# Kernel optimization log

Measured on AMD Instinct MI355X. Metric: run time of the kernel, lower is better.

Reference implementation:

```python
import jax, jax.numpy as jnp
import numpy as np

B, T, DIN, D = 32, 2048, 512, 512


def setup_inputs() -> dict:
    key = jax.random.key(0)
    k0, k1, k2, k3 = jax.random.split(key, 4)
    x = jax.random.normal(k0, (B, T, DIN), dtype=jnp.float32)
    h0 = jax.random.normal(k1, (B, D), dtype=jnp.float32)
    s0 = jax.random.normal(k2, (B, D), dtype=jnp.float32)
    # nn.Linear(input_dim, 6*hidden_dim): weight [6D, DIN], bias [6D]
    W = jax.random.normal(k3, (6 * D, DIN), dtype=jnp.float32) / np.float32(np.sqrt(DIN))
    b = jnp.zeros((6 * D,), dtype=jnp.float32)
    return {"x": x, "h0": h0, "s0": s0, "W": W, "b": b}


def reference(x, h0, s0, W, b):
    # Fused input projection for all 6 gates, done once as a big GEMM: [B,T,6D]
    proj = jnp.einsum("bti,oi->bto", x, W) + b
    proj = jnp.transpose(proj, (1, 0, 2))  # [T, B, 6D] for scan over time
    sig = jax.nn.sigmoid

    def step(carry, z):
        h, s = carry  # each [B, D]
        z0, z1, z2, z3, z4, z5 = jnp.split(z, 6, axis=-1)
        # gated two-state recurrence (6 gates, input-only projection,
        # elementwise recurrence on h/s as in the fused Triton cell)
        s_new = sig(z0) * s + sig(z1) * jnp.tanh(z2)
        h_new = sig(z3) * h + sig(z4) * jnp.tanh(z5 + s_new)
        return (h_new, s_new), h_new

    (hT, sT), hs = jax.lax.scan(step, (h0, s0), proj)
    out = jnp.transpose(hs, (1, 0, 2))  # [B, T, D]
    return out, sT
```

## Files before the change

kernel.cpp:

```cpp
#include <hip/hip_runtime.h>
#include <hip/hip_bf16.h>
#include <cstddef>
#include <cstdint>

#define BB   32
#define TT   2048
#define DIN  512
#define DD   512
#define NN   3072
#define PW   3072
#define PF   16

#define BMT 256
#define BNT 256
#define BKT 32
#define NKT (DIN / BKT)

typedef __attribute__((ext_vector_type(4))) float f32x4;
typedef __attribute__((ext_vector_type(8))) short s16x8;

__device__ __forceinline__ void gl2lds16(const void* g, void* l) {
    __builtin_amdgcn_global_load_lds(
        (const __attribute__((address_space(1))) unsigned*)g,
        (__attribute__((address_space(3))) unsigned*)l, 16, 0, 0);
}

__device__ __forceinline__ unsigned short bfr(float f) {
    unsigned u = __float_as_uint(f);
    u += 0x7fffu + ((u >> 16) & 1u);
    return (unsigned short)(u >> 16);
}

__device__ __forceinline__ float ftanh(float x) {
    return 1.f - 2.f * __builtin_amdgcn_rcpf(1.f + __builtin_amdgcn_exp2f(x * 2.885390082f));
}

__device__ __forceinline__ float h2lo(unsigned u) {
    return (float)__builtin_bit_cast(_Float16, (unsigned short)(u & 0xffffu));
}
__device__ __forceinline__ float h2hi(unsigned u) {
    return (float)__builtin_bit_cast(_Float16, (unsigned short)(u >> 16));
}

__global__ __launch_bounds__(256) void convert_x(
    const float* __restrict__ x, unsigned short* __restrict__ x2)
{
    const int total4 = BB * TT * DIN / 4;
    for (int idx = blockIdx.x * 256 + threadIdx.x; idx < total4;
         idx += gridDim.x * 256) {
        int e = idx * 4;
        int b = e >> 20;
        int t = (e >> 9) & 2047;
        int i = e & 511;
        float4 v = *(const float4*)(x + (size_t)e);
        ushort4 o;
        o.x = bfr(v.x); o.y = bfr(v.y); o.z = bfr(v.z); o.w = bfr(v.w);
        *(ushort4*)(x2 + ((size_t)((t << 5) | b) << 9) + i) = o;
    }
}

__global__ __launch_bounds__(128) void convert_w(
    const float* __restrict__ W, const float* __restrict__ bias,
    unsigned short* __restrict__ W2, float* __restrict__ bias2)
{
    int c = blockIdx.x;
    int p = c >> 10, d = (c & 1023) >> 1, q = c & 1;
    int o = ((2 * p + q) << 9) + d;
    const float* src = W + (size_t)o * DIN;
    unsigned short* dst = W2 + (size_t)c * DIN;
    int i = threadIdx.x * 4;
    float4 v = *(const float4*)(src + i);
    ushort4 u;
    u.x = bfr(v.x); u.y = bfr(v.y); u.z = bfr(v.z); u.w = bfr(v.w);
    *(ushort4*)(dst + i) = u;
    if (threadIdx.x == 0) bias2[c] = bias[o];
}

__global__ __launch_bounds__(512, 2) void gemm_proj10(
    const unsigned short* __restrict__ x2,
    const unsigned short* __restrict__ W2,
    const float* __restrict__ bias2,
    _Float16* __restrict__ proj,
    int t0)
{
    __shared__ unsigned short lds[3 * 16384];

    const unsigned nwg = gridDim.x;
    const unsigned fb  = blockIdx.x;
    const unsigned qq  = nwg >> 3, rr8 = nwg & 7;
    const unsigned xcd = fb & 7, sid = fb >> 3;
    const unsigned work = (xcd < rr8 ? xcd * (qq + 1)
                                     : rr8 * (qq + 1) + (xcd - rr8) * qq) + sid;
    const int bx = (int)(work % (NN / BNT));
    const int by = (int)(work / (NN / BNT));

    const int tid  = threadIdx.x;
    const int row0 = by * BMT;
    const int col0 = bx * BNT;
    const size_t growA = (size_t)t0 * BB + row0;

    const int lane = tid & 63;
    const int wv   = tid >> 6;
    const int wm   = wv >> 2;
    const int wn   = wv & 3;
    const int lr   = lane & 15;
    const int lq   = lane >> 4;

    auto stageA = [&](int s, int kt) {
        unsigned short* Ab = lds + s * 16384;
        const int k0 = kt * BKT;
        #pragma unroll
        for (int a = 0; a < 2; ++a) {
            int cid = a * 512 + tid;
            int rt  = cid >> 2;
            int cp  = cid & 3;
            gl2lds16(x2 + (growA + rt) * DIN + k0 + cp * 8, Ab + cid * 8);
        }
    };
    auto stageB = [&](int s, int kt) {
        unsigned short* Bb = lds + s * 16384 + 8192;
        const int k0 = kt * BKT;
        #pragma unroll
        for (int a = 0; a < 2; ++a) {
            int cid = a * 512 + tid;
            int rt  = cid >> 2;
            int cp  = cid & 3;
            gl2lds16(W2 + (size_t)(col0 + rt) * DIN + k0 + cp * 8, Bb + cid * 8);
        }
    };

    f32x4 acc[8][4] = {};

    stageA(0, 0); stageB(0, 0);
    stageA(1, 1); stageB(1, 1);
    asm volatile("s_waitcnt vmcnt(4)" ::: "memory");
    __builtin_amdgcn_s_barrier();

    #pragma unroll
    for (int kt = 0; kt < NKT; ++kt) {
        const unsigned short* Ab = lds + (kt % 3) * 16384;
        const unsigned short* Bb = Ab + 8192;
        const int  ks = (kt + 2) % 3;
        const bool st = (kt + 2) < NKT;

        if (st) { stageA(ks, kt + 2); stageB(ks, kt + 2); }

        s16x8 bv[4], av[8];
        #pragma unroll
        for (int j = 0; j < 4; ++j) {
            int col = wn * 64 + j * 16 + lr;
            bv[j] = *(const s16x8*)(Bb + col * BKT + lq * 8);
        }
        #pragma unroll
        for (int m = 0; m < 8; ++m) {
            int row = wm * 128 + m * 16 + lr;
            av[m] = *(const s16x8*)(Ab + row * BKT + lq * 8);
        }

        __builtin_amdgcn_s_setprio(1);
        #pragma unroll
        for (int m = 0; m < 8; ++m)
            #pragma unroll
            for (int j = 0; j < 4; ++j)
                acc[m][j] = __builtin_amdgcn_mfma_f32_16x16x32_bf16(
                    bv[j], av[m], acc[m][j], 0, 0, 0);
        __builtin_amdgcn_s_setprio(0);

        if (kt + 1 < NKT) {
            if (st) asm volatile("s_waitcnt vmcnt(4)" ::: "memory");
            else    asm volatile("s_waitcnt vmcnt(0)" ::: "memory");
            __builtin_amdgcn_s_barrier();
        }
    }

    const int p = col0 >> 10;
    const bool evenTanh = (p == 1);
    const bool oddIdent = (p == 2);
    const float mEven = evenTanh ? 2.885390082f : -1.442695041f;

    #pragma unroll
    for (int m = 0; m < 8; ++m) {
        int prow = row0 + wm * 128 + m * 16 + lr;
        _Float16* dst = proj + (size_t)prow * PW;
        #pragma unroll
        for (int j = 0; j < 4; ++j) {
            int cbase = col0 + wn * 64 + j * 16 + lq * 4;
            float4 bc = *(const float4*)(bias2 + cbase);
            float z0 = acc[m][j][0] + bc.x;
            float z1 = acc[m][j][1] + bc.y;
            float z2 = acc[m][j][2] + bc.z;
            float z3 = acc[m][j][3] + bc.w;
            float e0 = __builtin_amdgcn_rcpf(1.f + __builtin_amdgcn_exp2f(z0 * mEven));
            float e2 = __builtin_amdgcn_rcpf(1.f + __builtin_amdgcn_exp2f(z2 * mEven));
            float v0 = evenTanh ? (1.f - 2.f * e0) : e0;
            float v2 = evenTanh ? (1.f - 2.f * e2) : e2;
            float v1 = oddIdent ? z1
                : __builtin_amdgcn_rcpf(1.f + __builtin_amdgcn_exp2f(z1 * -1.442695041f));
            float v3 = oddIdent ? z3
                : __builtin_amdgcn_rcpf(1.f + __builtin_amdgcn_exp2f(z3 * -1.442695041f));
            ushort4 o;
            o.x = __builtin_bit_cast(unsigned short, (_Float16)v0);
            o.y = __builtin_bit_cast(unsigned short, (_Float16)v1);
            o.z = __builtin_bit_cast(unsigned short, (_Float16)v2);
            o.w = __builtin_bit_cast(unsigned short, (_Float16)v3);
            *(ushort4*)(dst + cbase) = o;
        }
    }
}

__global__ __launch_bounds__(64) void scan_chunk(
    const _Float16* __restrict__ proj,
    const float* __restrict__ h0, const float* __restrict__ s0,
    float* __restrict__ outH, float* __restrict__ outS,
    int t0, int Tc)
{
    const int gid = blockIdx.x * 64 + threadIdx.x;
    const int b   = gid >> 9;
    const int d   = gid & 511;

    float h, s;
    if (t0 == 0) { h = h0[gid]; s = s0[gid]; }
    else {
        h = outH[((size_t)b * TT + (t0 - 1)) * DD + d];
        s = outS[gid];
    }

    const unsigned* pu = (const unsigned*)(proj + (size_t)b * PW + d * 2);
    const size_t tstr = (size_t)BB * PW / 2;
    float* oH = outH + ((size_t)b * TT + t0) * DD + d;

    unsigned bufA[PF][3], bufB[PF][3];
    #pragma unroll
    for (int u = 0; u < PF; ++u)
        #pragma unroll
        for (int p = 0; p < 3; ++p)
            bufA[u][p] = pu[(size_t)u * tstr + p * 512];

    for (int tb = 0; tb < Tc; tb += 2 * PF) {
        #pragma unroll
        for (int u = 0; u < PF; ++u) {
            int t = tb + PF + u; if (t > Tc - 1) t = Tc - 1;
            #pragma unroll
            for (int p = 0; p < 3; ++p)
                bufB[u][p] = pu[(size_t)t * tstr + p * 512];
        }
        #pragma unroll
        for (int u = 0; u < PF; ++u) {
            float a0 = h2lo(bufA[u][0]), a1 = h2hi(bufA[u][0]);
            float t2 = h2lo(bufA[u][1]), a3 = h2hi(bufA[u][1]);
            float a4 = h2lo(bufA[u][2]), z5 = h2hi(bufA[u][2]);
            s = __builtin_fmaf(a0, s, a1 * t2);
            h = __builtin_fmaf(a3, h, a4 * ftanh(z5 + s));
            oH[(size_t)(tb + u) * DD] = h;
        }
        #pragma unroll
        for (int u = 0; u < PF; ++u) {
            int t = tb + 2 * PF + u; if (t > Tc - 1) t = Tc - 1;
            #pragma unroll
            for (int p = 0; p < 3; ++p)
                bufA[u][p] = pu[(size_t)t * tstr + p * 512];
        }
        #pragma unroll
        for (int u = 0; u < PF; ++u) {
            float a0 = h2lo(bufB[u][0]), a1 = h2hi(bufB[u][0]);
            float t2 = h2lo(bufB[u][1]), a3 = h2hi(bufB[u][1]);
            float a4 = h2lo(bufB[u][2]), z5 = h2hi(bufB[u][2]);
            s = __builtin_fmaf(a0, s, a1 * t2);
            h = __builtin_fmaf(a3, h, a4 * ftanh(z5 + s));
            oH[(size_t)(tb + PF + u) * DD] = h;
        }
    }

    outS[gid] = s;
}

extern "C" void kernel_launch(void* const* d_in, const int* in_sizes, int n_in,
                              void* d_out, int out_size, void* d_ws, size_t ws_size,
                              hipStream_t stream) {
    const float* x    = (const float*)d_in[0];
    const float* h0   = (const float*)d_in[1];
    const float* s0   = (const float*)d_in[2];
    const float* W    = (const float*)d_in[3];
    const float* bias = (const float*)d_in[4];

    float* outH = (float*)d_out;
    float* outS = outH + (size_t)BB * TT * DD;

    char* ws = (char*)d_ws;
    const size_t x2_bytes = (size_t)BB * TT * DIN * 2;
    const size_t w2_bytes = (size_t)NN * DIN * 2;
    const size_t b2_bytes = (size_t)NN * 4;
    unsigned short* x2    = (unsigned short*)ws;
    unsigned short* W2    = (unsigned short*)(ws + x2_bytes);
    float*          bias2 = (float*)(ws + x2_bytes + w2_bytes);
    _Float16*       proj  = (_Float16*)(ws + x2_bytes + w2_bytes + b2_bytes);

    const size_t fixed = x2_bytes + w2_bytes + b2_bytes;
    const size_t per_t = (size_t)BB * PW * 2;
    size_t avail = ws_size > fixed ? ws_size - fixed : 0;
    int TcMax = (int)(avail / per_t);
    if (TcMax > 512) TcMax = 512;
    TcMax &= ~31;
    if (TcMax < 32) TcMax = 32;

    convert_x<<<2048, 256, 0, stream>>>(x, x2);
    convert_w<<<NN, 128, 0, stream>>>(W, bias, W2, bias2);

    for (int t0 = 0; t0 < TT; t0 += TcMax) {
        int Tc = TT - t0;
        if (Tc > TcMax) Tc = TcMax;
        int nblk = (NN / BNT) * (Tc * BB / BMT);
        gemm_proj10<<<nblk, 512, 0, stream>>>(x2, W2, bias2, proj, t0);
        scan_chunk<<<(BB * DD) / 64, 64, 0, stream>>>(proj, h0, s0, outH, outS, t0, Tc);
    }
}
```

Measured before the change: 487.8 us.

## Shrink GEMM tile to 128x128 with 4 waves and XOR-swizzled LDS layout

Replaces the 256x256 tile, 8-wave projection GEMM with a 128x128 tile, 4-wave kernel that has a smaller LDS footprint and allows three blocks per CU. It also applies an XOR swizzle to the 16-byte chunk index in LDS, on both the global-to-LDS staging and the fragment reads, to reduce bank conflicts. The intent is more workgroups and better occupancy for the chunked GEMM. The cost is lower data reuse per tile, which means more global/L2 traffic per FLOP.

Result: slower. 518.3 us (+6.3%).

```diff
diff --git a/kernel.cpp b/kernel.cpp
--- a/kernel.cpp
+++ b/kernel.cpp
@@ -11,8 +11,8 @@
 #define PW   3072
 #define PF   16
 
-#define BMT 256
-#define BNT 256
+#define BMT 128
+#define BNT 128
 #define BKT 32
 #define NKT (DIN / BKT)
 
@@ -76,14 +76,14 @@
     if (threadIdx.x == 0) bias2[c] = bias[o];
 }
 
-__global__ __launch_bounds__(512, 2) void gemm_proj10(
+__global__ __launch_bounds__(256, 3) void gemm_proj11(
     const unsigned short* __restrict__ x2,
     const unsigned short* __restrict__ W2,
     const float* __restrict__ bias2,
     _Float16* __restrict__ proj,
     int t0)
 {
-    __shared__ unsigned short lds[3 * 16384];
+    __shared__ unsigned short lds[3 * 8192];
 
     const unsigned nwg = gridDim.x;
     const unsigned fb  = blockIdx.x;
@@ -101,69 +101,65 @@
 
     const int lane = tid & 63;
     const int wv   = tid >> 6;
-    const int wm   = wv >> 2;
-    const int wn   = wv & 3;
+    const int wr   = wv >> 1;
+    const int wc   = wv & 1;
     const int lr   = lane & 15;
     const int lq   = lane >> 4;
 
-    auto stageA = [&](int s, int kt) {
-        unsigned short* Ab = lds + s * 16384;
+    auto stage = [&](int s, int kt) {
+        unsigned short* Ab = lds + s * 8192;
+        unsigned short* Bb = Ab + 4096;
         const int k0 = kt * BKT;
         #pragma unroll
         for (int a = 0; a < 2; ++a) {
-            int cid = a * 512 + tid;
-            int rt  = cid >> 2;
-            int cp  = cid & 3;
-            gl2lds16(x2 + (growA + rt) * DIN + k0 + cp * 8, Ab + cid * 8);
+            int c  = a * 256 + tid;
+            int rt = c >> 2, cp = c & 3;
+            gl2lds16(x2 + (growA + rt) * DIN + k0 + ((cp ^ (rt & 3)) * 8),
+                     Ab + c * 8);
+        }
+        #pragma unroll
+        for (int a = 0; a < 2; ++a) {
+            int c  = a * 256 + tid;
+            int rt = c >> 2, cp = c & 3;
+            gl2lds16(W2 + (size_t)(col0 + rt) * DIN + k0 + ((cp ^ (rt & 3)) * 8),
+                     Bb + c * 8);
         }
     };
-    auto stageB = [&](int s, int kt) {
-        unsigned short* Bb = lds + s * 16384 + 8192;
-        const int k0 = kt * BKT;
-        #pragma unroll
-        for (int a = 0; a < 2; ++a) {
-            int cid = a * 512 + tid;
-            int rt  = cid >> 2;
-            int cp  = cid & 3;
-            gl2lds16(W2 + (size_t)(col0 + rt) * DIN + k0 + cp * 8, Bb + cid * 8);
-        }
-    };
-
-    f32x4 acc[8][4] = {};
-
-    stageA(0, 0); stageB(0, 0);
-    stageA(1, 1); stageB(1, 1);
+
+    f32x4 acc[4][4] = {};
+
+    stage(0, 0);
+    stage(1, 1);
     asm volatile("s_waitcnt vmcnt(4)" ::: "memory");
     __builtin_amdgcn_s_barrier();
 
     #pragma unroll
     for (int kt = 0; kt < NKT; ++kt) {
-        const unsigned short* Ab = lds + (kt % 3) * 16384;
-        const unsigned short* Bb = Ab + 8192;
-        const int  ks = (kt + 2) % 3;
+        const unsigned short* Ab = lds + (kt % 3) * 8192;
+        const unsigned short* Bb = Ab + 4096;
         const bool st = (kt + 2) < NKT;
 
-        if (st) { stageA(ks, kt + 2); stageB(ks, kt + 2); }
-
-        s16x8 bv[4], av[8];
+        if (st) stage((kt + 2) % 3, kt + 2);
+
+        s16x8 bv[4], av[4];
         #pragma unroll
         for (int j = 0; j < 4; ++j) {
-            int col = wn * 64 + j * 16 + lr;
-            bv[j] = *(const s16x8*)(Bb + col * BKT + lq * 8);
-        }
-        #pragma unroll
-        for (int m = 0; m < 8; ++m) {
-            int row = wm * 128 + m * 16 + lr;
-            av[m] = *(const s16x8*)(Ab + row * BKT + lq * 8);
+            int col = wc * 64 + j * 16 + lr;
+            bv[j] = *(const s16x8*)(Bb + col * BKT + ((lq ^ (col & 3)) * 8));
+        }
+        #pragma unroll
+        for (int i = 0; i < 4; ++i) {
+            int row = wr * 64 + i * 16 + lr;
+            av[i] = *(const s16x8*)(Ab + row * BKT + ((lq ^ (row & 3)) * 8));
         }
 
         __builtin_amdgcn_s_setprio(1);
         #pragma unroll
-        for (int m = 0; m < 8; ++m)
+        for (int i = 0; i < 4; ++i)
             #pragma unroll
             for (int j = 0; j < 4; ++j)
-                acc[m][j] = __builtin_amdgcn_mfma_f32_16x16x32_bf16(
-                    bv[j], av[m], acc[m][j], 0, 0, 0);
+                acc[i][j] = __builtin_amdgcn_mfma_f32_16x16x32_bf16(
+                    bv[j], av[i], acc[i][j], 0, 0, 0);
         __builtin_amdgcn_s_setprio(0);
 
         if (kt + 1 < NKT) {
@@ -179,17 +175,17 @@
     const float mEven = evenTanh ? 2.885390082f : -1.442695041f;
 
     #pragma unroll
-    for (int m = 0; m < 8; ++m) {
-        int prow = row0 + wm * 128 + m * 16 + lr;
+    for (int i = 0; i < 4; ++i) {
+        int prow = row0 + wr * 64 + i * 16 + lr;
         _Float16* dst = proj + (size_t)prow * PW;
         #pragma unroll
         for (int j = 0; j < 4; ++j) {
-            int cbase = col0 + wn * 64 + j * 16 + lq * 4;
+            int cbase = col0 + wc * 64 + j * 16 + lq * 4;
             float4 bc = *(const float4*)(bias2 + cbase);
-            float z0 = acc[m][j][0] + bc.x;
-            float z1 = acc[m][j][1] + bc.y;
-            float z2 = acc[m][j][2] + bc.z;
-            float z3 = acc[m][j][3] + bc.w;
+            float z0 = acc[i][j][0] + bc.x;
+            float z1 = acc[i][j][1] + bc.y;
+            float z2 = acc[i][j][2] + bc.z;
+            float z3 = acc[i][j][3] + bc.w;
             float e0 = __builtin_amdgcn_rcpf(1.f + __builtin_amdgcn_exp2f(z0 * mEven));
             float e2 = __builtin_amdgcn_rcpf(1.f + __builtin_amdgcn_exp2f(z2 * mEven));
             float v0 = evenTanh ? (1.f - 2.f * e0) : e0;
@@ -310,7 +306,7 @@
         int Tc = TT - t0;
         if (Tc > TcMax) Tc = TcMax;
         int nblk = (NN / BNT) * (Tc * BB / BMT);
-        gemm_proj10<<<nblk, 512, 0, stream>>>(x2, W2, bias2, proj, t0);
+        gemm_proj11<<<nblk, 256, 0, stream>>>(x2, W2, bias2, proj, t0);
         scan_chunk<<<(BB * DD) / 64, 64, 0, stream>>>(proj, h0, s0, outH, outS, t0, Tc);
     }
 }
```

## Overlap chunked scan with next chunk's GEMM in one fused launch

Applied to the files above, without the earlier changes.

Merges the projection GEMM and the recurrent scan into a single kernel. The first 32 blocks scan the previous chunk while the remaining blocks compute the next chunk's projection into a double-buffered workspace, so the latency-bound scan overlaps the compute-bound GEMM. The GEMM epilogue now stages fp16 outputs through LDS so global stores are full 16-byte row writes. In exchange the chunk size is halved to make room for two buffers, there is one extra launch, and the 512-thread scan blocks leave fewer scan waves spread across CUs.

Result: faster. 461.1 us (median of 3 runs) (-5.5%).

```diff
diff --git a/kernel.cpp b/kernel.cpp
--- a/kernel.cpp
+++ b/kernel.cpp
@@ -10,6 +10,7 @@
 #define NN   3072
 #define PW   3072
 #define PF   16
+#define SCANBLKS 32
 
 #define BMT 256
 #define BNT 256
@@ -76,17 +77,83 @@
     if (threadIdx.x == 0) bias2[c] = bias[o];
 }
 
-__global__ __launch_bounds__(512, 2) void gemm_proj10(
+__global__ __launch_bounds__(512, 2) void fused_chunk(
     const unsigned short* __restrict__ x2,
     const unsigned short* __restrict__ W2,
     const float* __restrict__ bias2,
-    _Float16* __restrict__ proj,
-    int t0)
+    _Float16* __restrict__ projDst,
+    const _Float16* __restrict__ projSrc,
+    const float* __restrict__ h0, const float* __restrict__ s0,
+    float* __restrict__ outH, float* __restrict__ outS,
+    int t0g, int Tcg, int t0s, int Tcs)
 {
     __shared__ unsigned short lds[3 * 16384];
 
-    const unsigned nwg = gridDim.x;
-    const unsigned fb  = blockIdx.x;
+    if (blockIdx.x < SCANBLKS) {
+        if (t0s < 0) return;
+        const int gid = blockIdx.x * 512 + threadIdx.x;
+        const int b   = gid >> 9;
+        const int d   = gid & 511;
+
+        float h, s;
+        if (t0s == 0) { h = h0[gid]; s = s0[gid]; }
+        else {
+            h = outH[((size_t)b * TT + (t0s - 1)) * DD + d];
+            s = outS[gid];
+        }
+
+        const unsigned* pu = (const unsigned*)(projSrc + (size_t)b * PW + d * 2);
+        const size_t tstr = (size_t)BB * PW / 2;
+        float* oH = outH + ((size_t)b * TT + t0s) * DD + d;
+
+        unsigned bufA[PF][3], bufB[PF][3];
+        #pragma unroll
+        for (int u = 0; u < PF; ++u)
+            #pragma unroll
+            for (int p = 0; p < 3; ++p)
+                bufA[u][p] = pu[(size_t)u * tstr + p * 512];
+
+        for (int tb = 0; tb < Tcs; tb += 2 * PF) {
+            #pragma unroll
+            for (int u = 0; u < PF; ++u) {
+                int t = tb + PF + u; if (t > Tcs - 1) t = Tcs - 1;
+                #pragma unroll
+                for (int p = 0; p < 3; ++p)
+                    bufB[u][p] = pu[(size_t)t * tstr + p * 512];
+            }
+            #pragma unroll
+            for (int u = 0; u < PF; ++u) {
+                float a0 = h2lo(bufA[u][0]), a1 = h2hi(bufA[u][0]);
+                float t2 = h2lo(bufA[u][1]), a3 = h2hi(bufA[u][1]);
+                float a4 = h2lo(bufA[u][2]), z5 = h2hi(bufA[u][2]);
+                s = __builtin_fmaf(a0, s, a1 * t2);
+                h = __builtin_fmaf(a3, h, a4 * ftanh(z5 + s));
+                oH[(size_t)(tb + u) * DD] = h;
+            }
+            #pragma unroll
+            for (int u = 0; u < PF; ++u) {
+                int t = tb + 2 * PF + u; if (t > Tcs - 1) t = Tcs - 1;
+                #pragma unroll
+                for (int p = 0; p < 3; ++p)
+                    bufA[u][p] = pu[(size_t)t * tstr + p * 512];
+            }
+            #pragma unroll
+            for (int u = 0; u < PF; ++u) {
+                float a0 = h2lo(bufB[u][0]), a1 = h2hi(bufB[u][0]);
+                float t2 = h2lo(bufB[u][1]), a3 = h2hi(bufB[u][1]);
+                float a4 = h2lo(bufB[u][2]), z5 = h2hi(bufB[u][2]);
+                s = __builtin_fmaf(a0, s, a1 * t2);
+                h = __builtin_fmaf(a3, h, a4 * ftanh(z5 + s));
+                oH[(size_t)(tb + PF + u) * DD] = h;
+            }
+        }
+        outS[gid] = s;
+        return;
+    }
+
+    if (t0g < 0) return;
+    const unsigned nwg = gridDim.x - SCANBLKS;
+    const unsigned fb  = blockIdx.x - SCANBLKS;
     const unsigned qq  = nwg >> 3, rr8 = nwg & 7;
     const unsigned xcd = fb & 7, sid = fb >> 3;
     const unsigned work = (xcd < rr8 ? xcd * (qq + 1)
@@ -97,7 +164,7 @@
     const int tid  = threadIdx.x;
     const int row0 = by * BMT;
     const int col0 = bx * BNT;
-    const size_t growA = (size_t)t0 * BB + row0;
+    const size_t growA = (size_t)t0g * BB + row0;
 
     const int lane = tid & 63;
     const int wv   = tid >> 6;
@@ -140,10 +207,9 @@
     for (int kt = 0; kt < NKT; ++kt) {
         const unsigned short* Ab = lds + (kt % 3) * 16384;
         const unsigned short* Bb = Ab + 8192;
-        const int  ks = (kt + 2) % 3;
         const bool st = (kt + 2) < NKT;
 
-        if (st) { stageA(ks, kt + 2); stageB(ks, kt + 2); }
+        if (st) { stageA((kt + 2) % 3, kt + 2); stageB((kt + 2) % 3, kt + 2); }
 
         s16x8 bv[4], av[8];
         #pragma unroll
@@ -178,14 +244,15 @@
     const bool oddIdent = (p == 2);
     const float mEven = evenTanh ? 2.885390082f : -1.442695041f;
 
+    char* epi = (char*)lds + 32768 + wv * 2304;
+    const int colw = col0 + wn * 64;
+    const int l8 = lane & 7, lh = lane >> 3;
+
     #pragma unroll
     for (int m = 0; m < 8; ++m) {
-        int prow = row0 + wm * 128 + m * 16 + lr;
-        _Float16* dst = proj + (size_t)prow * PW;
         #pragma unroll
         for (int j = 0; j < 4; ++j) {
-            int cbase = col0 + wn * 64 + j * 16 + lq * 4;
-            float4 bc = *(const float4*)(bias2 + cbase);
+            float4 bc = *(const float4*)(bias2 + colw + j * 16 + lq * 4);
             float z0 = acc[m][j][0] + bc.x;
             float z1 = acc[m][j][1] + bc.y;
             float z2 = acc[m][j][2] + bc.z;
@@ -203,75 +270,16 @@
             o.y = __builtin_bit_cast(unsigned short, (_Float16)v1);
             o.z = __builtin_bit_cast(unsigned short, (_Float16)v2);
             o.w = __builtin_bit_cast(unsigned short, (_Float16)v3);
-            *(ushort4*)(dst + cbase) = o;
-        }
-    }
-}
-
-__global__ __launch_bounds__(64) void scan_chunk(
-    const _Float16* __restrict__ proj,
-    const float* __restrict__ h0, const float* __restrict__ s0,
-    float* __restrict__ outH, float* __restrict__ outS,
-    int t0, int Tc)
-{
-    const int gid = blockIdx.x * 64 + threadIdx.x;
-    const int b   = gid >> 9;
-    const int d   = gid & 511;
-
-    float h, s;
-    if (t0 == 0) { h = h0[gid]; s = s0[gid]; }
-    else {
-        h = outH[((size_t)b * TT + (t0 - 1)) * DD + d];
-        s = outS[gid];
-    }
-
-    const unsigned* pu = (const unsigned*)(proj + (size_t)b * PW + d * 2);
-    const size_t tstr = (size_t)BB * PW / 2;
-    float* oH = outH + ((size_t)b * TT + t0) * DD + d;
-
-    unsigned bufA[PF][3], bufB[PF][3];
-    #pragma unroll
-    for (int u = 0; u < PF; ++u)
-        #pragma unroll
-        for (int p = 0; p < 3; ++p)
-            bufA[u][p] = pu[(size_t)u * tstr + p * 512];
-
-    for (int tb = 0; tb < Tc; tb += 2 * PF) {
-        #pragma unroll
-        for (int u = 0; u < PF; ++u) {
-            int t = tb + PF + u; if (t > Tc - 1) t = Tc - 1;
-            #pragma unroll
-            for (int p = 0; p < 3; ++p)
-                bufB[u][p] = pu[(size_t)t * tstr + p * 512];
-        }
-        #pragma unroll
-        for (int u = 0; u < PF; ++u) {
-            float a0 = h2lo(bufA[u][0]), a1 = h2hi(bufA[u][0]);
-            float t2 = h2lo(bufA[u][1]), a3 = h2hi(bufA[u][1]);
-            float a4 = h2lo(bufA[u][2]), z5 = h2hi(bufA[u][2]);
-            s = __builtin_fmaf(a0, s, a1 * t2);
-            h = __builtin_fmaf(a3, h, a4 * ftanh(z5 + s));
-            oH[(size_t)(tb + u) * DD] = h;
-        }
-        #pragma unroll
-        for (int u = 0; u < PF; ++u) {
-            int t = tb + 2 * PF + u; if (t > Tc - 1) t = Tc - 1;
-            #pragma unroll
-            for (int p = 0; p < 3; ++p)
-                bufA[u][p] = pu[(size_t)t * tstr + p * 512];
-        }
-        #pragma unroll
-        for (int u = 0; u < PF; ++u) {
-            float a0 = h2lo(bufB[u][0]), a1 = h2hi(bufB[u][0]);
-            float t2 = h2lo(bufB[u][1]), a3 = h2hi(bufB[u][1]);
-            float a4 = h2lo(bufB[u][2]), z5 = h2hi(bufB[u][2]);
-            s = __builtin_fmaf(a0, s, a1 * t2);
-            h = __builtin_fmaf(a3, h, a4 * ftanh(z5 + s));
-            oH[(size_t)(tb + PF + u) * DD] = h;
-        }
-    }
-
-    outS[gid] = s;
+            *(ushort4*)(epi + lr * 144 + j * 32 + lq * 8) = o;
+        }
+        #pragma unroll
+        for (int hh = 0; hh < 2; ++hh) {
+            int rr = hh * 8 + lh;
+            uint4 v = *(const uint4*)(epi + rr * 144 + l8 * 16);
+            int g = row0 + wm * 128 + m * 16 + rr;
+            *(uint4*)((char*)projDst + ((size_t)g * PW + colw + l8 * 8) * 2) = v;
+        }
+    }
 }
 
 extern "C" void kernel_launch(void* const* d_in, const int* in_sizes, int n_in,
@@ -293,24 +301,39 @@
     unsigned short* x2    = (unsigned short*)ws;
     unsigned short* W2    = (unsigned short*)(ws + x2_bytes);
     float*          bias2 = (float*)(ws + x2_bytes + w2_bytes);
-    _Float16*       proj  = (_Float16*)(ws + x2_bytes + w2_bytes + b2_bytes);
 
     const size_t fixed = x2_bytes + w2_bytes + b2_bytes;
     const size_t per_t = (size_t)BB * PW * 2;
     size_t avail = ws_size > fixed ? ws_size - fixed : 0;
-    int TcMax = (int)(avail / per_t);
+    int TcMax = (int)(avail / (2 * per_t));
     if (TcMax > 512) TcMax = 512;
     TcMax &= ~31;
     if (TcMax < 32) TcMax = 32;
 
+    _Float16* projA = (_Float16*)(ws + fixed);
+    _Float16* projB = projA + (size_t)TcMax * BB * PW;
+
     convert_x<<<2048, 256, 0, stream>>>(x, x2);
     convert_w<<<NN, 128, 0, stream>>>(W, bias, W2, bias2);
 
-    for (int t0 = 0; t0 < TT; t0 += TcMax) {
-        int Tc = TT - t0;
-        if (Tc > TcMax) Tc = TcMax;
-        int nblk = (NN / BNT) * (Tc * BB / BMT);
-        gemm_proj10<<<nblk, 512, 0, stream>>>(x2, W2, bias2, proj, t0);
-        scan_chunk<<<(BB * DD) / 64, 64, 0, stream>>>(proj, h0, s0, outH, outS, t0, Tc);
-    }
-}
+    const int nC = (TT + TcMax - 1) / TcMax;
+    int prevT0 = -1, prevTc = 0;
+    const _Float16* prevProj = nullptr;
+
+    for (int ci = 0; ci <= nC; ++ci) {
+        const bool hasG = (ci < nC);
+        int t0 = ci * TcMax;
+        int Tc = 0;
+        _Float16* dst = nullptr;
+        int nG = 0;
+        if (hasG) {
+            Tc  = TT - t0; if (Tc > TcMax) Tc = TcMax;
+            dst = (ci & 1) ? projB : projA;
+            nG  = (NN / BNT) * (Tc * BB / BMT);
+        }
+        fused_chunk<<<dim3(SCANBLKS + nG), 512, 0, stream>>>(
+            x2, W2, bias2, dst, prevProj, h0, s0, outH, outS,
+            hasG ? t0 : -1, Tc, prevT0, prevTc);
+        if (hasG) { prevProj = dst; prevT0 = t0; prevTc = Tc; }
+    }
+}
```
